# Kernel tuning notes

Measured on AMD Instinct MI355X. Metric: run time of the kernel, lower is better.

## Reference

```python
import jax, jax.numpy as jnp
import numpy as np

N_NODES = 100000
N_EDGES = 3200000
IN_DIM = 128
EMB = 32
NUM_GRAPHS = 256


def setup_inputs() -> dict:
    key = jax.random.key(0)
    ks = jax.random.split(key, 7)
    x = jax.random.normal(ks[0], (N_NODES, IN_DIM), dtype=jnp.float32)
    edge_index = jax.random.randint(ks[1], (2, N_EDGES), 0, N_NODES, dtype=jnp.int64)
    batch_index = jnp.sort(jax.random.randint(ks[2], (N_NODES,), 0, NUM_GRAPHS, dtype=jnp.int64))
    W1 = jax.random.normal(ks[3], (IN_DIM, EMB), dtype=jnp.float32) * (1.0 / np.sqrt(IN_DIM))
    b1 = jax.random.normal(ks[4], (EMB,), dtype=jnp.float32) * 0.01
    Wout = jax.random.normal(ks[5], (2 * EMB, 1), dtype=jnp.float32) * (1.0 / np.sqrt(2 * EMB))
    bout = jax.random.normal(ks[6], (1,), dtype=jnp.float32) * 0.01
    return {"x": x, "edge_index": edge_index, "batch_index": batch_index,
            "W1": W1, "b1": b1, "Wout": Wout, "bout": bout}


def gcn_conv(x, edge_index, W, b):
    """PyG GCNConv: add self-loops, symmetric deg^-1/2 normalization, XW, scatter-add, +bias."""
    N = x.shape[0]
    xw = x @ W  # [N, out]
    src, dst = edge_index[0], edge_index[1]
    # degree includes self-loop (+1)
    deg = jax.ops.segment_sum(jnp.ones(src.shape[0], dtype=xw.dtype), dst, num_segments=N) + 1.0
    dinv = jax.lax.rsqrt(deg)  # deg >= 1 so safe
    norm = dinv[src] * dinv[dst]  # [E]
    msg = xw[src] * norm[:, None]  # [E, out]
    agg = jax.ops.segment_sum(msg, dst, num_segments=N)
    # self-loop contribution: dinv[i]^2 * xw[i]
    agg = agg + xw * (dinv * dinv)[:, None]
    return agg + b


def reference(x, edge_index, batch_index, W1, b1, Wout, bout):
    h = gcn_conv(x, edge_index, W1, b1)           # [N, EMB]
    h = jnp.tanh(h)
    sums = jax.ops.segment_sum(h, batch_index, num_segments=NUM_GRAPHS)   # global_add_pool
    counts = jax.ops.segment_sum(jnp.ones((h.shape[0],), dtype=h.dtype), batch_index, num_segments=NUM_GRAPHS)
    means = sums / jnp.maximum(counts, 1.0)[:, None]                       # global_mean_pool
    pooled = jnp.concatenate([sums, means], axis=1)  # [G, 2*EMB]
    return pooled @ Wout + bout                      # [G, 1]
```

## Files before the change

kernel.cpp:

```cpp
#include <hip/hip_runtime.h>
#include <hip/hip_fp16.h>

#define N_NODES    100000
#define N_EDGES    3200000
#define IN_DIM     128
#define EMB        32
#define NUM_GRAPHS 256

#define FB         1024
#define NODES_PB   128
#define NBUCKETS   782
#define FB_B       512
#define FB_EPB     6250
#define NCHUNK     16
#define CHROWS     32
#define XW_BLOCKS  1563
#define CAP        5632

typedef _Float16 half8 __attribute__((ext_vector_type(8)));
typedef float floatx4 __attribute__((ext_vector_type(4)));

__global__ __launch_bounds__(512) void k_hist(const int* __restrict__ ei,
                                              int* __restrict__ bhist) {
    __shared__ int h[FB];
    int t = threadIdx.x;
    for (int i = t; i < FB; i += 512) h[i] = 0;
    __syncthreads();
    int e0 = blockIdx.x * FB_EPB;
    for (int e = e0 + t; e < e0 + FB_EPB; e += 512)
        atomicAdd(&h[ei[N_EDGES + e] >> 7], 1);
    __syncthreads();
    for (int i = t; i < FB; i += 512) bhist[blockIdx.x * FB + i] = h[i];
}

__global__ __launch_bounds__(512) void k_part(const int* __restrict__ bhist,
                                              int* __restrict__ part,
                                              const int* __restrict__ batch,
                                              float* __restrict__ sums,
                                              float* __restrict__ counts) {
    int j = blockIdx.x, t = threadIdx.x;
    if (j == NCHUNK) {
        for (int i = t; i < NUM_GRAPHS * EMB; i += 512) sums[i] = 0.f;
        if (t < NUM_GRAPHS) {
            int lo = 0, hi = N_NODES;
            while (lo < hi) { int mid = (lo + hi) >> 1; if (batch[mid] < t) lo = mid + 1; else hi = mid; }
            int a = lo;
            lo = 0; hi = N_NODES;
            int g1 = t + 1;
            while (lo < hi) { int mid = (lo + hi) >> 1; if (batch[mid] < g1) lo = mid + 1; else hi = mid; }
            counts[t] = (float)(lo - a);
        }
        return;
    }
    int row0 = j * CHROWS;
    for (int b = t; b < FB; b += 512) {
        int acc = 0;
#pragma unroll 8
        for (int i = 0; i < CHROWS; ++i) acc += bhist[(row0 + i) * FB + b];
        part[j * FB + b] = acc;
    }
}

__global__ __launch_bounds__(1024) void k_mid(const int* __restrict__ bhist,
                                              const int* __restrict__ part,
                                              int* __restrict__ bbase,
                                              int* __restrict__ cbase) {
    __shared__ int ts[FB];
    int b = threadIdx.x;
    int j = blockIdx.x;
    int tot = 0;
#pragma unroll
    for (int k = 0; k < NCHUNK; ++k) tot += part[k * FB + b];
    ts[b] = tot;
    __syncthreads();
    for (int off = 1; off < FB; off <<= 1) {
        int u = (b >= off) ? ts[b - off] : 0;
        __syncthreads();
        ts[b] += u;
        __syncthreads();
    }
    int cb = ts[b] - tot;
    if (j == 0) {
        cbase[b] = cb;
        if (b == 0) cbase[FB] = N_EDGES;
    }
    int run = cb;
    for (int k = 0; k < j; ++k) run += part[k * FB + b];
    int row0 = j * CHROWS;
    for (int i = 0; i < CHROWS; ++i) {
        int h = bhist[(row0 + i) * FB + b];
        bbase[(row0 + i) * FB + b] = run;
        run += h;
    }
}

__global__ __launch_bounds__(512) void k_fill(const int* __restrict__ ei,
                                              const int* __restrict__ bhist,
                                              const int* __restrict__ bbase,
                                              unsigned int* __restrict__ recs) {
    __shared__ unsigned int staged[FB_EPB];
    __shared__ int dpos[FB_EPB];
    __shared__ int hd[FB];
    __shared__ int cur[FB];
    __shared__ int ts[512];
    int t = threadIdx.x;
    int rowoff = blockIdx.x * FB;
    for (int i = t; i < FB; i += 512) hd[i] = bhist[rowoff + i];
    __syncthreads();
    int v0 = hd[2 * t], v1 = hd[2 * t + 1];
    int tot = v0 + v1;
    ts[t] = tot;
    __syncthreads();
    for (int off = 1; off < 512; off <<= 1) {
        int u = (t >= off) ? ts[t - off] : 0;
        __syncthreads();
        ts[t] += u;
        __syncthreads();
    }
    int lb0 = ts[t] - tot;
    int lb1 = lb0 + v0;
    cur[2 * t] = lb0;
    cur[2 * t + 1] = lb1;
    hd[2 * t]     = bbase[rowoff + 2 * t]     - lb0;
    hd[2 * t + 1] = bbase[rowoff + 2 * t + 1] - lb1;
    __syncthreads();
    int e0 = blockIdx.x * FB_EPB;
    for (int e = e0 + t; e < e0 + FB_EPB; e += 512) {
        int s = ei[e];
        int d = ei[N_EDGES + e];
        int b = d >> 7;
        int lpos = atomicAdd(&cur[b], 1);
        staged[lpos] = ((unsigned int)(d & 127) << 24) | (unsigned int)s;
        dpos[lpos] = lpos + hd[b];
    }
    __syncthreads();
    for (int j = t; j < FB_EPB; j += 512)
        recs[dpos[j]] = staged[j];
}

__global__ __launch_bounds__(512) void k_fill2(const unsigned int* __restrict__ recs,
                                               const int* __restrict__ cbase,
                                               int* __restrict__ edge_src,
                                               int* __restrict__ rowstart,
                                               float* __restrict__ dinv) {
    __shared__ unsigned int lbuf[CAP];
    __shared__ int h2[NODES_PB], cur2[NODES_PB], sc[NODES_PB];
    int t = threadIdx.x, b = blockIdx.x;
    if (t < NODES_PB) h2[t] = 0;
    __syncthreads();
    int seg0 = cbase[b];
    int cnt = cbase[b + 1] - seg0;
    for (int j = t; j < cnt; j += 512) {
        unsigned int r = recs[seg0 + j];
        if (j < CAP) lbuf[j] = r;
        atomicAdd(&h2[r >> 24], 1);
    }
    __syncthreads();
    int v = 0;
    if (t < NODES_PB) { v = h2[t]; sc[t] = v; }
    __syncthreads();
    for (int off = 1; off < NODES_PB; off <<= 1) {
        int u = 0;
        if (t < NODES_PB && t >= off) u = sc[t - off];
        __syncthreads();
        if (t < NODES_PB) sc[t] += u;
        __syncthreads();
    }
    int node0 = b << 7;
    if (t < NODES_PB) {
        int excl = sc[t] - v;
        cur2[t] = excl;
        int node = node0 + t;
        if (node < N_NODES) {
            rowstart[node] = seg0 + excl;
            dinv[node] = rsqrtf((float)v + 1.0f);
        }
    }
    if (b == 0 && t == 0) rowstart[N_NODES] = N_EDGES;
    __syncthreads();
    for (int j = t; j < cnt; j += 512) {
        unsigned int r = (j < CAP) ? lbuf[j] : recs[seg0 + j];
        int p = atomicAdd(&cur2[r >> 24], 1);
        edge_src[seg0 + p] = (int)(r & 0x00FFFFFF);
    }
}

__global__ __launch_bounds__(256) void k_xw(const float* __restrict__ x,
                                            const float* __restrict__ W1,
                                            const float* __restrict__ dinv,
                                            __half* __restrict__ xwh) {
    __shared__ _Float16 Wh[IN_DIM * (EMB + 1)];
    for (int i = threadIdx.x; i < IN_DIM * EMB; i += 256)
        Wh[(i >> 5) * (EMB + 1) + (i & 31)] = (_Float16)W1[i];
    __syncthreads();
    int wave = threadIdx.x >> 6;
    int lane = threadIdx.x & 63;
    int m = lane & 15, quad = lane >> 4;
    int row0 = (blockIdx.x * 4 + wave) * 16;
    if (row0 >= N_NODES) return;
    half8 bfrag[2][4];
#pragma unroll
    for (int nt = 0; nt < 2; ++nt)
#pragma unroll
        for (int ks = 0; ks < 4; ++ks)
#pragma unroll
            for (int j = 0; j < 8; ++j)
                bfrag[nt][ks][j] = Wh[(ks * 32 + quad * 8 + j) * (EMB + 1) + nt * 16 + m];
    const float* xr = x + (size_t)(row0 + m) * IN_DIM + quad * 8;
    floatx4 c0 = {0.f, 0.f, 0.f, 0.f}, c1 = {0.f, 0.f, 0.f, 0.f};
#pragma unroll
    for (int ks = 0; ks < 4; ++ks) {
        float4 a0 = *(const float4*)(xr + ks * 32);
        float4 a1 = *(const float4*)(xr + ks * 32 + 4);
        half8 af;
        af[0] = (_Float16)a0.x; af[1] = (_Float16)a0.y;
        af[2] = (_Float16)a0.z; af[3] = (_Float16)a0.w;
        af[4] = (_Float16)a1.x; af[5] = (_Float16)a1.y;
        af[6] = (_Float16)a1.z; af[7] = (_Float16)a1.w;
        c0 = __builtin_amdgcn_mfma_f32_16x16x32_f16(af, bfrag[0][ks], c0, 0, 0, 0);
        c1 = __builtin_amdgcn_mfma_f32_16x16x32_f16(af, bfrag[1][ks], c1, 0, 0, 0);
    }
#pragma unroll
    for (int r = 0; r < 4; ++r) {
        int ro = row0 + quad * 4 + r;
        float di = dinv[ro];
        xwh[(size_t)ro * EMB + m]      = __float2half(c0[r] * di);
        xwh[(size_t)ro * EMB + 16 + m] = __float2half(c1[r] * di);
    }
}

template<int K>
__device__ __forceinline__ void gstep(const int* __restrict__ es,
                                      const float2* __restrict__ rows8,
                                      int cc, int e,
                                      float& a0, float& a1, float& a2, float& a3) {
    int s[K];
    float2 f[K];
#pragma unroll
    for (int k = 0; k < K; ++k) s[k] = es[e + k];
#pragma unroll
    for (int k = 0; k < K; ++k) f[k] = rows8[(size_t)s[k] * 8 + cc];
#pragma unroll
    for (int k = 0; k < K; ++k) {
        float2 g01 = __half22float2(*(const __half2*)&f[k].x);
        float2 g23 = __half22float2(*(const __half2*)&f[k].y);
        a0 += g01.x; a1 += g01.y; a2 += g23.x; a3 += g23.y;
    }
}

__global__ __launch_bounds__(256) void k_gather(const __half* __restrict__ xws,
                                                const float* __restrict__ dinv,
                                                const int* __restrict__ rowstart,
                                                const int* __restrict__ edge_src,
                                                const int* __restrict__ batch,
                                                const float* __restrict__ b1,
                                                float* __restrict__ sums) {
    const float2* rows8 = (const float2*)xws;
    int grp = threadIdx.x >> 3;
    int cc  = threadIdx.x & 7;
    int i = blockIdx.x * 32 + grp;
    float di = dinv[i];
    int e0 = rowstart[i], e1 = rowstart[i + 1];
    float a0 = 0.f, a1 = 0.f, a2 = 0.f, a3 = 0.f;
    int e = e0;
    for (; e + 8 <= e1; e += 8) gstep<8>(edge_src, rows8, cc, e, a0, a1, a2, a3);
    if (e + 4 <= e1) { gstep<4>(edge_src, rows8, cc, e, a0, a1, a2, a3); e += 4; }
    if (e + 2 <= e1) { gstep<2>(edge_src, rows8, cc, e, a0, a1, a2, a3); e += 2; }
    if (e < e1)      { gstep<1>(edge_src, rows8, cc, e, a0, a1, a2, a3); }
    float2 fr = rows8[(size_t)i * 8 + cc];
    float2 fs01 = __half22float2(*(const __half2*)&fr.x);
    float2 fs23 = __half22float2(*(const __half2*)&fr.y);
    float4 bb = *(const float4*)(b1 + 4 * cc);
    float h0 = tanhf((a0 + fs01.x) * di + bb.x);
    float h1 = tanhf((a1 + fs01.y) * di + bb.y);
    float h2 = tanhf((a2 + fs23.x) * di + bb.z);
    float h3 = tanhf((a3 + fs23.y) * di + bb.w);

    __shared__ float hs[32][EMB];
    __shared__ int gb[32];
    *(float4*)&hs[grp][4 * cc] = make_float4(h0, h1, h2, h3);
    if (cc == 0) gb[grp] = batch[i];
    __syncthreads();
    if (threadIdx.x < 32) {
        int col = threadIdx.x;
        int rr = 0;
        while (rr < 32) {
            int g0 = gb[rr];
            float a = hs[rr][col];
            int r2 = rr + 1;
            while (r2 < 32 && gb[r2] == g0) { a += hs[r2][col]; ++r2; }
            atomicAdd(&sums[g0 * EMB + col], a);
            rr = r2;
        }
    }
}

__global__ __launch_bounds__(64) void k_out(const float* __restrict__ sums,
                                            const float* __restrict__ counts,
                                            const float* __restrict__ Wout,
                                            const float* __restrict__ bout,
                                            float* __restrict__ out) {
    int g = blockIdx.x * 64 + threadIdx.x;
    if (g >= NUM_GRAPHS) return;
    float inv = 1.0f / fmaxf(counts[g], 1.0f);
    float acc = bout[0];
#pragma unroll
    for (int c = 0; c < EMB; ++c) {
        float s = sums[g * EMB + c];
        acc += s * Wout[c] + s * inv * Wout[EMB + c];
    }
    out[g] = acc;
}

extern "C" void kernel_launch(void* const* d_in, const int* in_sizes, int n_in,
                              void* d_out, int out_size, void* d_ws, size_t ws_size,
                              hipStream_t stream) {
    const float* x     = (const float*)d_in[0];
    const int*   ei    = (const int*)d_in[1];
    const int*   batch = (const int*)d_in[2];
    const float* W1    = (const float*)d_in[3];
    const float* b1    = (const float*)d_in[4];
    const float* Wout  = (const float*)d_in[5];
    const float* bout  = (const float*)d_in[6];
    float* out = (float*)d_out;

    char* ws = (char*)d_ws;
    __half* xwh        = (__half*)ws;       ws += (size_t)N_NODES * EMB * sizeof(__half);
    unsigned int* recs = (unsigned int*)ws; ws += (size_t)N_EDGES * sizeof(int);
    int*   edge_src    = (int*)ws;          ws += (size_t)N_EDGES * sizeof(int);
    int*   rowstart    = (int*)ws;          ws += (size_t)(N_NODES + 4) * sizeof(int);
    float* dinv        = (float*)ws;        ws += (size_t)N_NODES * sizeof(float);
    int*   cbase       = (int*)ws;          ws += (FB + 2) * sizeof(int);
    float* sums        = (float*)ws;        ws += (size_t)NUM_GRAPHS * EMB * sizeof(float);
    float* counts      = (float*)ws;

    int* bhist = edge_src;
    int* part  = bhist + (size_t)FB_B * FB;
    int* bbase = part + (size_t)NCHUNK * FB;

    k_hist  <<<FB_B, 512, 0, stream>>>(ei, bhist);
    k_part  <<<NCHUNK + 1, 512, 0, stream>>>(bhist, part, batch, sums, counts);
    k_mid   <<<NCHUNK, 1024, 0, stream>>>(bhist, part, bbase, cbase);
    k_fill  <<<FB_B, 512, 0, stream>>>(ei, bhist, bbase, recs);
    k_fill2 <<<NBUCKETS, 512, 0, stream>>>(recs, cbase, edge_src, rowstart, dinv);
    k_xw    <<<XW_BLOCKS, 256, 0, stream>>>(x, W1, dinv, xwh);
    k_gather<<<N_NODES / 32, 256, 0, stream>>>(xwh, dinv, rowstart, edge_src, batch, b1, sums);
    k_out   <<<(NUM_GRAPHS + 63) / 64, 64, 0, stream>>>(sums, counts, Wout, bout, out);
}
```

Before: 209.5 us.

## Replace two-level bucket sort CSR build with global-atomic counting sort

The multi-pass bucketed CSR construction (histogram, partial sums, mid scan, staged fill, per-bucket fill) is replaced by a direct counting sort. Global atomics compute per-node degree, a two-kernel tile scan produces rowstart and cursor arrays, and a placement kernel scatters source indices with global atomics on the cursors. This removes several kernels and the intermediate record buffer, but relies on contended global atomics and random scattered writes. Edge loads also use nontemporal hints.

Measured after the change: 581.3 us. 2.78x slower.

```diff
diff --git a/kernel.cpp b/kernel.cpp
--- a/kernel.cpp
+++ b/kernel.cpp
@@ -7,40 +7,59 @@
 #define EMB        32
 #define NUM_GRAPHS 256
 
-#define FB         1024
-#define NODES_PB   128
-#define NBUCKETS   782
-#define FB_B       512
-#define FB_EPB     6250
-#define NCHUNK     16
-#define CHROWS     32
-#define XW_BLOCKS  1563
-#define CAP        5632
+#define EDGE_BLOCKS 1563
+#define STILE       1024
+#define SBLK        98
+#define XW_BLOCKS   1563
 
 typedef _Float16 half8 __attribute__((ext_vector_type(8)));
 typedef float floatx4 __attribute__((ext_vector_type(4)));
-
-__global__ __launch_bounds__(512) void k_hist(const int* __restrict__ ei,
-                                              int* __restrict__ bhist) {
-    __shared__ int h[FB];
-    int t = threadIdx.x;
-    for (int i = t; i < FB; i += 512) h[i] = 0;
-    __syncthreads();
-    int e0 = blockIdx.x * FB_EPB;
-    for (int e = e0 + t; e < e0 + FB_EPB; e += 512)
-        atomicAdd(&h[ei[N_EDGES + e] >> 7], 1);
-    __syncthreads();
-    for (int i = t; i < FB; i += 512) bhist[blockIdx.x * FB + i] = h[i];
-}
-
-__global__ __launch_bounds__(512) void k_part(const int* __restrict__ bhist,
-                                              int* __restrict__ part,
-                                              const int* __restrict__ batch,
-                                              float* __restrict__ sums,
-                                              float* __restrict__ counts) {
-    int j = blockIdx.x, t = threadIdx.x;
-    if (j == NCHUNK) {
-        for (int i = t; i < NUM_GRAPHS * EMB; i += 512) sums[i] = 0.f;
+typedef int intx4 __attribute__((ext_vector_type(4)));
+
+__global__ __launch_bounds__(512) void k_deg(const int* __restrict__ ei,
+                                             int* __restrict__ deg) {
+    int idx = blockIdx.x * 512 + threadIdx.x;
+    int e = idx * 4;
+    if (e < N_EDGES) {
+        intx4 d4 = __builtin_nontemporal_load((const intx4*)(ei + N_EDGES + e));
+        atomicAdd(&deg[d4.x], 1);
+        atomicAdd(&deg[d4.y], 1);
+        atomicAdd(&deg[d4.z], 1);
+        atomicAdd(&deg[d4.w], 1);
+    }
+}
+
+__global__ __launch_bounds__(256) void k_sa(const int* __restrict__ deg,
+                                            int* __restrict__ tsum) {
+    __shared__ int red[256];
+    int b = blockIdx.x, t = threadIdx.x;
+    int base = b * STILE + t * 4;
+    int s = 0;
+#pragma unroll
+    for (int q = 0; q < 4; ++q) {
+        int i = base + q;
+        if (i < N_NODES) s += deg[i];
+    }
+    red[t] = s;
+    __syncthreads();
+    for (int off = 128; off; off >>= 1) {
+        if (t < off) red[t] += red[t + off];
+        __syncthreads();
+    }
+    if (t == 0) tsum[b] = red[0];
+}
+
+__global__ __launch_bounds__(256) void k_sb(const int* __restrict__ deg,
+                                            const int* __restrict__ tsum,
+                                            int* __restrict__ rowstart,
+                                            int* __restrict__ cur,
+                                            float* __restrict__ dinv,
+                                            const int* __restrict__ batch,
+                                            float* __restrict__ sums,
+                                            float* __restrict__ counts) {
+    int b = blockIdx.x, t = threadIdx.x;
+    if (b == SBLK) {
+        for (int i = t; i < NUM_GRAPHS * EMB; i += 256) sums[i] = 0.f;
         if (t < NUM_GRAPHS) {
             int lo = 0, hi = N_NODES;
             while (lo < hi) { int mid = (lo + hi) >> 1; if (batch[mid] < t) lo = mid + 1; else hi = mid; }
@@ -50,138 +69,60 @@
             while (lo < hi) { int mid = (lo + hi) >> 1; if (batch[mid] < g1) lo = mid + 1; else hi = mid; }
             counts[t] = (float)(lo - a);
         }
+        if (t == 0) rowstart[N_NODES] = N_EDGES;
         return;
     }
-    int row0 = j * CHROWS;
-    for (int b = t; b < FB; b += 512) {
-        int acc = 0;
-#pragma unroll 8
-        for (int i = 0; i < CHROWS; ++i) acc += bhist[(row0 + i) * FB + b];
-        part[j * FB + b] = acc;
-    }
-}
-
-__global__ __launch_bounds__(1024) void k_mid(const int* __restrict__ bhist,
-                                              const int* __restrict__ part,
-                                              int* __restrict__ bbase,
-                                              int* __restrict__ cbase) {
-    __shared__ int ts[FB];
-    int b = threadIdx.x;
-    int j = blockIdx.x;
-    int tot = 0;
-#pragma unroll
-    for (int k = 0; k < NCHUNK; ++k) tot += part[k * FB + b];
-    ts[b] = tot;
-    __syncthreads();
-    for (int off = 1; off < FB; off <<= 1) {
-        int u = (b >= off) ? ts[b - off] : 0;
+    __shared__ int pre[128];
+    __shared__ int ts2[256];
+    __shared__ int off_s;
+    if (t < SBLK) pre[t] = tsum[t];
+    int base = b * STILE + t * 4;
+    int d[4]; int ssum = 0;
+#pragma unroll
+    for (int q = 0; q < 4; ++q) {
+        int i = base + q;
+        d[q] = (i < N_NODES) ? deg[i] : 0;
+        ssum += d[q];
+    }
+    __syncthreads();
+    if (t == 0) { int o = 0; for (int k = 0; k < b; ++k) o += pre[k]; off_s = o; }
+    ts2[t] = ssum;
+    __syncthreads();
+    for (int off = 1; off < 256; off <<= 1) {
+        int u = (t >= off) ? ts2[t - off] : 0;
         __syncthreads();
-        ts[b] += u;
+        ts2[t] += u;
         __syncthreads();
     }
-    int cb = ts[b] - tot;
-    if (j == 0) {
-        cbase[b] = cb;
-        if (b == 0) cbase[FB] = N_EDGES;
-    }
-    int run = cb;
-    for (int k = 0; k < j; ++k) run += part[k * FB + b];
-    int row0 = j * CHROWS;
-    for (int i = 0; i < CHROWS; ++i) {
-        int h = bhist[(row0 + i) * FB + b];
-        bbase[(row0 + i) * FB + b] = run;
-        run += h;
-    }
-}
-
-__global__ __launch_bounds__(512) void k_fill(const int* __restrict__ ei,
-                                              const int* __restrict__ bhist,
-                                              const int* __restrict__ bbase,
-                                              unsigned int* __restrict__ recs) {
-    __shared__ unsigned int staged[FB_EPB];
-    __shared__ int dpos[FB_EPB];
-    __shared__ int hd[FB];
-    __shared__ int cur[FB];
-    __shared__ int ts[512];
-    int t = threadIdx.x;
-    int rowoff = blockIdx.x * FB;
-    for (int i = t; i < FB; i += 512) hd[i] = bhist[rowoff + i];
-    __syncthreads();
-    int v0 = hd[2 * t], v1 = hd[2 * t + 1];
-    int tot = v0 + v1;
-    ts[t] = tot;
-    __syncthreads();
-    for (int off = 1; off < 512; off <<= 1) {
-        int u = (t >= off) ? ts[t - off] : 0;
-        __syncthreads();
-        ts[t] += u;
-        __syncthreads();
-    }
-    int lb0 = ts[t] - tot;
-    int lb1 = lb0 + v0;
-    cur[2 * t] = lb0;
-    cur[2 * t + 1] = lb1;
-    hd[2 * t]     = bbase[rowoff + 2 * t]     - lb0;
-    hd[2 * t + 1] = bbase[rowoff + 2 * t + 1] - lb1;
-    __syncthreads();
-    int e0 = blockIdx.x * FB_EPB;
-    for (int e = e0 + t; e < e0 + FB_EPB; e += 512) {
-        int s = ei[e];
-        int d = ei[N_EDGES + e];
-        int b = d >> 7;
-        int lpos = atomicAdd(&cur[b], 1);
-        staged[lpos] = ((unsigned int)(d & 127) << 24) | (unsigned int)s;
-        dpos[lpos] = lpos + hd[b];
-    }
-    __syncthreads();
-    for (int j = t; j < FB_EPB; j += 512)
-        recs[dpos[j]] = staged[j];
-}
-
-__global__ __launch_bounds__(512) void k_fill2(const unsigned int* __restrict__ recs,
-                                               const int* __restrict__ cbase,
-                                               int* __restrict__ edge_src,
-                                               int* __restrict__ rowstart,
-                                               float* __restrict__ dinv) {
-    __shared__ unsigned int lbuf[CAP];
-    __shared__ int h2[NODES_PB], cur2[NODES_PB], sc[NODES_PB];
-    int t = threadIdx.x, b = blockIdx.x;
-    if (t < NODES_PB) h2[t] = 0;
-    __syncthreads();
-    int seg0 = cbase[b];
-    int cnt = cbase[b + 1] - seg0;
-    for (int j = t; j < cnt; j += 512) {
-        unsigned int r = recs[seg0 + j];
-        if (j < CAP) lbuf[j] = r;
-        atomicAdd(&h2[r >> 24], 1);
-    }
-    __syncthreads();
-    int v = 0;
-    if (t < NODES_PB) { v = h2[t]; sc[t] = v; }
-    __syncthreads();
-    for (int off = 1; off < NODES_PB; off <<= 1) {
-        int u = 0;
-        if (t < NODES_PB && t >= off) u = sc[t - off];
-        __syncthreads();
-        if (t < NODES_PB) sc[t] += u;
-        __syncthreads();
-    }
-    int node0 = b << 7;
-    if (t < NODES_PB) {
-        int excl = sc[t] - v;
-        cur2[t] = excl;
-        int node = node0 + t;
-        if (node < N_NODES) {
-            rowstart[node] = seg0 + excl;
-            dinv[node] = rsqrtf((float)v + 1.0f);
+    int run = off_s + ts2[t] - ssum;
+#pragma unroll
+    for (int q = 0; q < 4; ++q) {
+        int i = base + q;
+        if (i < N_NODES) {
+            rowstart[i] = run;
+            cur[i] = run;
+            dinv[i] = rsqrtf((float)d[q] + 1.0f);
         }
-    }
-    if (b == 0 && t == 0) rowstart[N_NODES] = N_EDGES;
-    __syncthreads();
-    for (int j = t; j < cnt; j += 512) {
-        unsigned int r = (j < CAP) ? lbuf[j] : recs[seg0 + j];
-        int p = atomicAdd(&cur2[r >> 24], 1);
-        edge_src[seg0 + p] = (int)(r & 0x00FFFFFF);
+        run += d[q];
+    }
+}
+
+__global__ __launch_bounds__(512) void k_place(const int* __restrict__ ei,
+                                               int* __restrict__ cur,
+                                               int* __restrict__ edge_src) {
+    int idx = blockIdx.x * 512 + threadIdx.x;
+    int e = idx * 4;
+    if (e < N_EDGES) {
+        intx4 s4 = __builtin_nontemporal_load((const intx4*)(ei + e));
+        intx4 d4 = __builtin_nontemporal_load((const intx4*)(ei + N_EDGES + e));
+        int p0 = atomicAdd(&cur[d4.x], 1);
+        int p1 = atomicAdd(&cur[d4.y], 1);
+        int p2 = atomicAdd(&cur[d4.z], 1);
+        int p3 = atomicAdd(&cur[d4.w], 1);
+        edge_src[p0] = s4.x;
+        edge_src[p1] = s4.y;
+        edge_src[p2] = s4.z;
+        edge_src[p3] = s4.w;
     }
 }
 
@@ -237,7 +178,7 @@
     int s[K];
     float2 f[K];
 #pragma unroll
-    for (int k = 0; k < K; ++k) s[k] = es[e + k];
+    for (int k = 0; k < K; ++k) s[k] = __builtin_nontemporal_load(es + e + k);
 #pragma unroll
     for (int k = 0; k < K; ++k) f[k] = rows8[(size_t)s[k] * 8 + cc];
 #pragma unroll
@@ -325,24 +266,22 @@
     float* out = (float*)d_out;
 
     char* ws = (char*)d_ws;
-    __half* xwh        = (__half*)ws;       ws += (size_t)N_NODES * EMB * sizeof(__half);
-    unsigned int* recs = (unsigned int*)ws; ws += (size_t)N_EDGES * sizeof(int);
-    int*   edge_src    = (int*)ws;          ws += (size_t)N_EDGES * sizeof(int);
-    int*   rowstart    = (int*)ws;          ws += (size_t)(N_NODES + 4) * sizeof(int);
-    float* dinv        = (float*)ws;        ws += (size_t)N_NODES * sizeof(float);
-    int*   cbase       = (int*)ws;          ws += (FB + 2) * sizeof(int);
-    float* sums        = (float*)ws;        ws += (size_t)NUM_GRAPHS * EMB * sizeof(float);
-    float* counts      = (float*)ws;
-
-    int* bhist = edge_src;
-    int* part  = bhist + (size_t)FB_B * FB;
-    int* bbase = part + (size_t)NCHUNK * FB;
-
-    k_hist  <<<FB_B, 512, 0, stream>>>(ei, bhist);
-    k_part  <<<NCHUNK + 1, 512, 0, stream>>>(bhist, part, batch, sums, counts);
-    k_mid   <<<NCHUNK, 1024, 0, stream>>>(bhist, part, bbase, cbase);
-    k_fill  <<<FB_B, 512, 0, stream>>>(ei, bhist, bbase, recs);
-    k_fill2 <<<NBUCKETS, 512, 0, stream>>>(recs, cbase, edge_src, rowstart, dinv);
+    __half* xwh     = (__half*)ws; ws += (size_t)N_NODES * EMB * sizeof(__half);
+    int* edge_src   = (int*)ws;    ws += (size_t)N_EDGES * sizeof(int);
+    int* rowstart   = (int*)ws;    ws += (size_t)(N_NODES + 4) * sizeof(int);
+    int* cur        = (int*)ws;    ws += (size_t)N_NODES * sizeof(int);
+    int* deg        = (int*)ws;    ws += (size_t)N_NODES * sizeof(int);
+    float* dinv     = (float*)ws;  ws += (size_t)N_NODES * sizeof(float);
+    int* tsum       = (int*)ws;    ws += 128 * sizeof(int);
+    float* sums     = (float*)ws;  ws += (size_t)NUM_GRAPHS * EMB * sizeof(float);
+    float* counts   = (float*)ws;
+
+    hipMemsetAsync(deg, 0, (size_t)N_NODES * sizeof(int), stream);
+
+    k_deg   <<<EDGE_BLOCKS, 512, 0, stream>>>(ei, deg);
+    k_sa    <<<SBLK, 256, 0, stream>>>(deg, tsum);
+    k_sb    <<<SBLK + 1, 256, 0, stream>>>(deg, tsum, rowstart, cur, dinv, batch, sums, counts);
+    k_place <<<EDGE_BLOCKS, 512, 0, stream>>>(ei, cur, edge_src);
     k_xw    <<<XW_BLOCKS, 256, 0, stream>>>(x, W1, dinv, xwh);
     k_gather<<<N_NODES / 32, 256, 0, stream>>>(xwh, dinv, rowstart, edge_src, batch, b1, sums);
     k_out   <<<(NUM_GRAPHS + 63) / 64, 64, 0, stream>>>(sums, counts, Wout, bout, out);
```
